# Optimization experiments

Hardware: AMD Instinct MI355X
Metric: run time of the kernel (lower is better)

## Reference

```python
import jax, jax.numpy as jnp
import numpy as np

H = W = 512
IN_DIM = 3
WIDTH = 64
N_LAYERS = 4
M1 = M2 = 20
FC_DIM = 128
OUT_DIM = 1


def setup_inputs() -> dict:
    key = jax.random.key(0)
    ks = jax.random.split(key, 12)
    s = 1.0 / (WIDTH * WIDTH)
    return {
        "x": jax.random.normal(ks[0], (H, W, IN_DIM), jnp.float32),
        "fc0_w": jax.random.normal(ks[1], (WIDTH, IN_DIM), jnp.float32) * 0.1,
        "fc0_b": jnp.zeros((WIDTH,), jnp.float32),
        "sw1_r": jax.random.normal(ks[2], (N_LAYERS, WIDTH, WIDTH, M1, M2), jnp.float32) * s,
        "sw1_i": jax.random.normal(ks[3], (N_LAYERS, WIDTH, WIDTH, M1, M2), jnp.float32) * s,
        "sw2_r": jax.random.normal(ks[4], (N_LAYERS, WIDTH, WIDTH, M1, M2), jnp.float32) * s,
        "sw2_i": jax.random.normal(ks[5], (N_LAYERS, WIDTH, WIDTH, M1, M2), jnp.float32) * s,
        "conv_w": jax.random.normal(ks[6], (N_LAYERS, WIDTH, WIDTH), jnp.float32) * 0.1,
        "conv_b": jnp.zeros((N_LAYERS, WIDTH), jnp.float32),
        "fc1_w": jax.random.normal(ks[7], (FC_DIM, WIDTH), jnp.float32) * 0.1,
        "fc1_b": jnp.zeros((FC_DIM,), jnp.float32),
        "fc2_w": jax.random.normal(ks[8], (OUT_DIM, FC_DIM), jnp.float32) * 0.1,
        "fc2_b": jnp.zeros((OUT_DIM,), jnp.float32),
    }


def _spectral_conv(v, w1, w2):
    # v: (C, H, W); w1, w2: (C_in, C_out, M1, M2) complex64
    xf = jnp.fft.rfft2(v)  # (C, H, W//2+1) complex64
    out_ft = jnp.zeros((w1.shape[1], H, W // 2 + 1), jnp.complex64)
    top = jnp.einsum("ixy,ioxy->oxy", xf[:, :M1, :M2], w1)
    bot = jnp.einsum("ixy,ioxy->oxy", xf[:, -M1:, :M2], w2)
    out_ft = out_ft.at[:, :M1, :M2].set(top).at[:, -M1:, :M2].set(bot)
    return jnp.fft.irfft2(out_ft, s=(H, W))


def reference(x, fc0_w, fc0_b, sw1_r, sw1_i, sw2_r, sw2_i, conv_w, conv_b,
              fc1_w, fc1_b, fc2_w, fc2_b):
    v = jnp.transpose(x, (2, 0, 1))  # (in_dim, H, W)
    # fc0 applied pointwise over the grid (double_vmap Linear on channel axis)
    v = jnp.einsum("chw,oc->ohw", v, fc0_w) + fc0_b[:, None, None]
    for i in range(N_LAYERS):
        w1 = (sw1_r[i] + 1j * sw1_i[i]).astype(jnp.complex64)
        w2 = (sw2_r[i] + 1j * sw2_i[i]).astype(jnp.complex64)
        x1 = _spectral_conv(v, w1, w2)
        x2 = jnp.einsum("chw,oc->ohw", v, conv_w[i]) + conv_b[i][:, None, None]
        v = jnp.tanh(x1 + x2)
    v = jnp.tanh(jnp.einsum("chw,oc->ohw", v, fc1_w) + fc1_b[:, None, None])
    v = jnp.einsum("chw,oc->ohw", v, fc2_w) + fc2_b[:, None, None]
    return jnp.transpose(v, (1, 2, 0))  # (H, W, out_dim)
```

## Files before the change

### kernel.cpp

```cpp
#include <hip/hip_runtime.h>
#include <math.h>

typedef unsigned short u16;
typedef __attribute__((ext_vector_type(8))) short short8;
typedef __attribute__((ext_vector_type(8))) short bf16x8;
typedef __attribute__((ext_vector_type(4))) unsigned short us4;
typedef __attribute__((ext_vector_type(2))) unsigned short us2;
typedef __attribute__((ext_vector_type(8))) unsigned short us8;
typedef __attribute__((ext_vector_type(4))) float f32x4;

#define NP (512*512)
#define MFMA16 __builtin_amdgcn_mfma_f32_16x16x32_bf16

#define TWH   0u
#define TWL   49152u
#define T2H   98304u
#define T2L   163840u
#define THC2H 229376u
#define THC2L 278528u
#define THS2H 327680u
#define THS2L 376832u
#define THCAH 425984u
#define THCAL 491520u
#define THSAH 557056u
#define THSAL 622592u
#define THSNH 688128u
#define THSNL 753664u
#define CFH   819200u
#define CFL   851968u
#define F1H   884736u
#define F1L   901120u
#define XWH   917504u
#define XWL   4063232u
#define XFP   7208960u
#define YPART 8028160u
#define YRH   8847360u
#define YRL   9011200u
#define YIH   9175040u
#define YIL   9338880u
#define ZH    9502720u
#define ZL    13697024u
#define VH    17891328u
#define VL    51445760u

__device__ __forceinline__ u16 brnd(float x){
    unsigned u = __float_as_uint(x);
    unsigned r = (u + 0x7FFFu + ((u>>16)&1u)) >> 16;
    return (u16)r;
}
__device__ __forceinline__ float fbf(u16 h){ return __uint_as_float(((unsigned)h)<<16); }
__device__ __forceinline__ void bsplit(float x, u16& h, u16& l){
    h = brnd(x); l = brnd(x - fbf(h));
}
__device__ __forceinline__ float tanhfast(float x){
    x = fminf(10.f, fmaxf(-10.f, x));
    float e = __expf(2.f*x);
    return (e-1.f)/(e+1.f);
}

__global__ void k_setup(char* wsb, const float* __restrict__ convw, const float* __restrict__ fc1w){
    int i = blockIdx.x*256 + threadIdx.x;
    const float c2pi = 6.283185307179586f/512.0f;
    if (i < 24576){
        int e=i&7, lane=(i>>3)&63, g=i>>9; int nt=g%3;
        int k = (g/3)*32 + ((lane>>4)<<3) + e;
        int n = nt*16 + (lane&15);
        float v=0.f;
        if(n<40){int kx=n>>1; float a=c2pi*(float)((kx*k)&511); v=(n&1)?-sinf(a):cosf(a);}
        u16 h,l; bsplit(v,h,l);
        ((u16*)(wsb+TWH))[i]=h; ((u16*)(wsb+TWL))[i]=l;
    } else if (i < 57344){
        int j2=i-24576;
        int e=j2&7, lane=(j2>>3)&63, g=j2>>9; int ks=g&1, wt=g>>1;
        int j = ks*32 + ((lane>>4)<<3) + e;
        int w = wt*16 + (lane&15);
        float v=0.f;
        if(j<40){int kx=j>>1; float a=c2pi*(float)((kx*w)&511); v=(j&1)?-sinf(a):cosf(a);}
        u16 h,l; bsplit(v,h,l);
        ((u16*)(wsb+T2H))[j2]=h; ((u16*)(wsb+T2L))[j2]=l;
    } else if (i < 81920){
        int j2 = i-57344;
        int m=j2>>9, hh=j2&511;
        float vc=0.f,vs=0.f;
        if(m<40){int ky=(m<20)?m:(472+m); float a=c2pi*(float)((ky*hh)&511); vc=cosf(a); vs=sinf(a);}
        u16 h,l;
        bsplit(vc,h,l); ((u16*)(wsb+THC2H))[j2]=h; ((u16*)(wsb+THC2L))[j2]=l;
        bsplit(vs,h,l); ((u16*)(wsb+THS2H))[j2]=h; ((u16*)(wsb+THS2L))[j2]=l;
    } else if (i < 114688){
        int j2 = i-81920;
        int hh=j2>>6, m=j2&63;
        float vc=0.f,vs=0.f;
        if(m<40){int ky=(m<20)?m:(472+m); float a=c2pi*(float)((ky*hh)&511); vc=cosf(a); vs=sinf(a);}
        u16 h,l;
        bsplit(vc,h,l);  ((u16*)(wsb+THCAH))[j2]=h; ((u16*)(wsb+THCAL))[j2]=l;
        bsplit(vs,h,l);  ((u16*)(wsb+THSAH))[j2]=h; ((u16*)(wsb+THSAL))[j2]=l;
        bsplit(-vs,h,l); ((u16*)(wsb+THSNH))[j2]=h; ((u16*)(wsb+THSNL))[j2]=l;
    } else {
        int j = i - 114688;
        if (j < 16384){
            int e=j&7, lane=(j>>3)&63, g=j>>9;
            int mt=g&3, ks=(g>>2)&1, L=g>>3;
            int o = mt*16+(lane&15), c = ks*32+((lane>>4)<<3)+e;
            float v = convw[L*4096 + o*64 + c];
            u16 h,l; bsplit(v,h,l);
            ((u16*)(wsb+CFH))[j]=h; ((u16*)(wsb+CFL))[j]=l;
        } else {
            int j2=j-16384;
            int e=j2&7, lane=(j2>>3)&63, g=j2>>9;
            int mt=g&7, ks=g>>3;
            int f = mt*16+(lane&15), c = ks*32+((lane>>4)<<3)+e;
            float v = fc1w[f*64+c];
            u16 h,l; bsplit(v,h,l);
            ((u16*)(wsb+F1H))[j2]=h; ((u16*)(wsb+F1L))[j2]=l;
        }
    }
}

__global__ __launch_bounds__(256) void k_fc0(const float* __restrict__ x,
    const float* __restrict__ w, const float* __restrict__ b,
    u16* __restrict__ vh, u16* __restrict__ vl){
    __shared__ float xs[1024*3];
    __shared__ float ws3[192], bs[64];
    int t = threadIdx.x;
    size_t pb = (size_t)blockIdx.x*1024;
    const float4* xg = (const float4*)(x + pb*3);
    float4* xs4 = (float4*)xs;
    #pragma unroll
    for (int k=0;k<3;k++) xs4[t + k*256] = xg[t + k*256];
    if (t<192) ws3[t]=w[t];
    if (t<64) bs[t]=b[t];
    __syncthreads();
    int p0 = t*4;
    float X0[4],X1[4],X2[4];
    #pragma unroll
    for(int e=0;e<4;e++){X0[e]=xs[(p0+e)*3];X1[e]=xs[(p0+e)*3+1];X2[e]=xs[(p0+e)*3+2];}
    for (int c=0;c<64;c++){
        float w0=ws3[c*3],w1=ws3[c*3+1],w2=ws3[c*3+2],bc=bs[c];
        us4 sh, sl;
        #pragma unroll
        for(int e=0;e<4;e++){
            float v = w0*X0[e]+w1*X1[e]+w2*X2[e]+bc;
            u16 hh,ll; bsplit(v,hh,ll); sh[e]=hh; sl[e]=ll;
        }
        *(us4*)(vh + (size_t)c*NP + pb + p0) = sh;
        *(us4*)(vl + (size_t)c*NP + pb + p0) = sl;
    }
}

__global__ __launch_bounds__(256) void k_f1(const u16* __restrict__ vh, const u16* __restrict__ vl,
    const u16* __restrict__ twh, const u16* __restrict__ twl,
    u16* __restrict__ xwh, u16* __restrict__ xwl){
    int lane = threadIdx.x & 63, wv = threadIdx.x >> 6;
    int rowa = blockIdx.x*64 + wv*16 + (lane&15);
    const u16* ah = vh + (size_t)rowa*512 + ((lane>>4)<<3);
    const u16* al = vl + (size_t)rowa*512 + ((lane>>4)<<3);
    f32x4 acc[3];
    #pragma unroll
    for (int nt = 0; nt < 3; ++nt) acc[nt] = (f32x4){0.f,0.f,0.f,0.f};
    #pragma unroll 2
    for (int kk = 0; kk < 16; ++kk){
        bf16x8 Ah = *reinterpret_cast<const bf16x8*>(ah + kk*32);
        bf16x8 Al = *reinterpret_cast<const bf16x8*>(al + kk*32);
        bf16x8 Bh[3], Bl[3];
        #pragma unroll
        for (int nt = 0; nt < 3; ++nt){
            size_t bo = ((size_t)(kk*3+nt)*64 + lane)*8;
            Bh[nt] = *reinterpret_cast<const bf16x8*>(twh + bo);
            Bl[nt] = *reinterpret_cast<const bf16x8*>(twl + bo);
        }
        #pragma unroll
        for (int nt = 0; nt < 3; ++nt){
            acc[nt] = MFMA16(Ah, Bh[nt], acc[nt], 0,0,0);
            acc[nt] = MFMA16(Ah, Bl[nt], acc[nt], 0,0,0);
            acc[nt] = MFMA16(Al, Bh[nt], acc[nt], 0,0,0);
        }
    }
    int r0 = blockIdx.x*64 + wv*16 + ((lane>>4)<<2);
    int c = r0>>9, h0 = r0&511;
    int colj = lane&15;
    #pragma unroll
    for (int nt = 0; nt < 3; ++nt){
        int j = nt*16 + colj;
        us4 uh, ul;
        #pragma unroll
        for (int rg = 0; rg < 4; ++rg){
            u16 hh,ll; bsplit(acc[nt][rg],hh,ll); uh[rg]=hh; ul[rg]=ll;
        }
        size_t off = ((size_t)j*64 + c)*512 + h0;
        *(us4*)(xwh + off) = uh;
        *(us4*)(xwl + off) = ul;
    }
}

__global__ __launch_bounds__(256) void k_f2(const char* __restrict__ wsb, float* __restrict__ xfP){
    int b = blockIdx.x;
    int kx = b/6, r = b%6, mt = r>>1, kh = r&1;
    int lane = threadIdx.x&63, wv = threadIdx.x>>6;
    const u16* thch=(const u16*)(wsb+THC2H); const u16* thcl=(const u16*)(wsb+THC2L);
    const u16* thsh=(const u16*)(wsb+THS2H); const u16* thsl=(const u16*)(wsb+THS2L);
    const u16* xwh=(const u16*)(wsb+XWH);   const u16* xwl=(const u16*)(wsb+XWL);
    f32x4 aA=(f32x4){0,0,0,0}, aB=aA, aC=aA, aD=aA;
    int g8 = (lane>>4)<<3;
    int mrow = lane&15;
    int cB = wv*16 + (lane&15);
    size_t bre = ((size_t)(2*kx)*64 + cB)*512;
    size_t bim = ((size_t)(2*kx+1)*64 + cB)*512;
    for (int kk = kh*8; kk < kh*8+8; ++kk){
        int hof = kk*32 + g8;
        bf16x8 XRh = *reinterpret_cast<const bf16x8*>(xwh + bre + hof);
        bf16x8 XRl = *reinterpret_cast<const bf16x8*>(xwl + bre + hof);
        bf16x8 XIh = *reinterpret_cast<const bf16x8*>(xwh + bim + hof);
        bf16x8 XIl = *reinterpret_cast<const bf16x8*>(xwl + bim + hof);
        size_t ao = (size_t)(mt*16+mrow)*512 + hof;
        bf16x8 Ch = *reinterpret_cast<const bf16x8*>(thch+ao);
        bf16x8 Cl = *reinterpret_cast<const bf16x8*>(thcl+ao);
        bf16x8 Sh = *reinterpret_cast<const bf16x8*>(thsh+ao);
        bf16x8 Sl = *reinterpret_cast<const bf16x8*>(thsl+ao);
        aA=MFMA16(Ch,XRh,aA,0,0,0); aA=MFMA16(Ch,XRl,aA,0,0,0); aA=MFMA16(Cl,XRh,aA,0,0,0);
        aB=MFMA16(Sh,XIh,aB,0,0,0); aB=MFMA16(Sh,XIl,aB,0,0,0); aB=MFMA16(Sl,XIh,aB,0,0,0);
        aC=MFMA16(Ch,XIh,aC,0,0,0); aC=MFMA16(Ch,XIl,aC,0,0,0); aC=MFMA16(Cl,XIh,aC,0,0,0);
        aD=MFMA16(Sh,XRh,aD,0,0,0); aD=MFMA16(Sh,XRl,aD,0,0,0); aD=MFMA16(Sl,XRh,aD,0,0,0);
    }
    #pragma unroll
    for (int rg=0;rg<4;rg++){
        int m = mt*16 + ((lane>>4)<<2) + rg;
        if (m < 40){
            float re = aA[rg]+aB[rg];
            float im = aC[rg]-aD[rg];
            size_t xo = ((size_t)kh*64 + cB)*1600 + (size_t)(m*20+kx)*2;
            xfP[xo] = re; xfP[xo+1] = im;
        }
    }
}

__global__ __launch_bounds__(256) void k_mix(const float* __restrict__ w1r,const float* __restrict__ w1i,
    const float* __restrict__ w2r,const float* __restrict__ w2i,
    const float* __restrict__ xfP, float* __restrict__ ypart){
    __shared__ float xs[2][800];
    int b = blockIdx.x;
    int iseg = b>>7, half = (b>>6)&1, o = b&63;
    int t = threadIdx.x;
    const float* wr = (half? w2r : w1r) + o*400;
    const float* wi = (half? w2i : w1i) + o*400;
    const float* xp0 = xfP + half*800;
    const float* xp1 = xfP + (size_t)64*1600 + half*800;
    int i0 = iseg*32;
    {
        const float* a = xp0 + (size_t)i0*1600; const float* c = xp1 + (size_t)i0*1600;
        xs[0][t]=a[t]+c[t]; xs[0][t+256]=a[t+256]+c[t+256];
        if (t<288) xs[0][t+512]=a[t+512]+c[t+512];
    }
    int p1 = t, p2 = t+256; bool has2 = (p2<400);
    float ar1=0,ai1=0,ar2=0,ai2=0;
    size_t wof = (size_t)i0*25600;
    float wAr1=wr[wof+p1], wAi1=wi[wof+p1];
    float wAr2=0,wAi2=0;
    if(has2){ wAr2=wr[wof+p2]; wAi2=wi[wof+p2]; }
    __syncthreads();
    for (int ii=0; ii<32; ++ii){
        int cur = ii&1;
        if (ii<31){
            int i = i0+ii+1;
            const float* a = xp0 + (size_t)i*1600; const float* c = xp1 + (size_t)i*1600;
            float* d = xs[cur^1];
            d[t]=a[t]+c[t]; d[t+256]=a[t+256]+c[t+256];
            if(t<288) d[t+512]=a[t+512]+c[t+512];
        }
        float wBr1=0,wBi1=0,wBr2=0,wBi2=0;
        if (ii<31){
            size_t wo2 = (size_t)(i0+ii+1)*25600;
            wBr1=wr[wo2+p1]; wBi1=wi[wo2+p1];
            if(has2){ wBr2=wr[wo2+p2]; wBi2=wi[wo2+p2]; }
        }
        float xr=xs[cur][2*p1], xi=xs[cur][2*p1+1];
        ar1 += xr*wAr1 - xi*wAi1; ai1 += xr*wAi1 + xi*wAr1;
        if (has2){
            float xr2=xs[cur][2*p2], xi2=xs[cur][2*p2+1];
            ar2 += xr2*wAr2 - xi2*wAi2; ai2 += xr2*wAi2 + xi2*wAr2;
        }
        wAr1=wBr1; wAi1=wBi1; wAr2=wBr2; wAi2=wBi2;
        __syncthreads();
    }
    int mode1 = half*400 + p1;
    size_t y1 = ((size_t)(iseg*800 + mode1)*64 + o)*2;
    ypart[y1]=ar1; ypart[y1+1]=ai1;
    if (has2){
        int mode2 = half*400 + p2;
        size_t y2 = ((size_t)(iseg*800 + mode2)*64 + o)*2;
        ypart[y2]=ar2; ypart[y2+1]=ai2;
    }
}

__global__ void k_mixred(const float* __restrict__ ypart, char* wsb){
    int g = blockIdx.x*256+threadIdx.x;
    int m = g&63, o=(g>>6)&63, kx=g>>12;
    float vr=0.f, vi=0.f;
    if (m<40){
        int mode = m*20+kx;
        size_t i0 = ((size_t)mode*64+o)*2;
        size_t i1 = ((size_t)(800+mode)*64+o)*2;
        float sc = (kx==0?1.f:2.f)*(1.f/262144.f);
        vr = (ypart[i0]+ypart[i1])*sc;
        vi = (ypart[i0+1]+ypart[i1+1])*sc;
    }
    u16 h,l; size_t yo = ((size_t)kx*64+o)*64+m;
    bsplit(vr,h,l); ((u16*)(wsb+YRH))[yo]=h; ((u16*)(wsb+YRL))[yo]=l;
    bsplit(vi,h,l); ((u16*)(wsb+YIH))[yo]=h; ((u16*)(wsb+YIL))[yo]=l;
}

__global__ __launch_bounds__(128) void k_i1(const char* __restrict__ wsb,
    u16* __restrict__ zh, u16* __restrict__ zl){
    int b = blockIdx.x; int kx = b>>4, hb = b&15;
    int lane = threadIdx.x&63, wv = threadIdx.x>>6;
    const u16* thcAh=(const u16*)(wsb+THCAH); const u16* thcAl=(const u16*)(wsb+THCAL);
    const u16* thsAh=(const u16*)(wsb+THSAH); const u16* thsAl=(const u16*)(wsb+THSAL);
    const u16* thsnh=(const u16*)(wsb+THSNH); const u16* thsnl=(const u16*)(wsb+THSNL);
    const u16* yrh=(const u16*)(wsb+YRH); const u16* yrl=(const u16*)(wsb+YRL);
    const u16* yih=(const u16*)(wsb+YIH); const u16* yil=(const u16*)(wsb+YIL);
    f32x4 aR[4], aI[4];
    #pragma unroll
    for(int nt=0;nt<4;nt++){aR[nt]=(f32x4){0,0,0,0}; aI[nt]=aR[nt];}
    int g8 = (lane>>4)<<3;
    int hrow = hb*32 + wv*16 + (lane&15);
    #pragma unroll
    for (int ks=0; ks<2; ++ks){
        size_t ao = (size_t)hrow*64 + ks*32 + g8;
        bf16x8 Ch=*reinterpret_cast<const bf16x8*>(thcAh+ao);
        bf16x8 Cl=*reinterpret_cast<const bf16x8*>(thcAl+ao);
        bf16x8 Sh=*reinterpret_cast<const bf16x8*>(thsAh+ao);
        bf16x8 Sl=*reinterpret_cast<const bf16x8*>(thsAl+ao);
        bf16x8 Nh=*reinterpret_cast<const bf16x8*>(thsnh+ao);
        bf16x8 Nl=*reinterpret_cast<const bf16x8*>(thsnl+ao);
        #pragma unroll
        for (int nt=0; nt<4; ++nt){
            int o = nt*16+(lane&15);
            size_t bo = ((size_t)kx*64+o)*64 + ks*32 + g8;
            bf16x8 Rh=*reinterpret_cast<const bf16x8*>(yrh+bo);
            bf16x8 Rl=*reinterpret_cast<const bf16x8*>(yrl+bo);
            bf16x8 Ih=*reinterpret_cast<const bf16x8*>(yih+bo);
            bf16x8 Il=*reinterpret_cast<const bf16x8*>(yil+bo);
            aR[nt]=MFMA16(Ch,Rh,aR[nt],0,0,0); aR[nt]=MFMA16(Ch,Rl,aR[nt],0,0,0); aR[nt]=MFMA16(Cl,Rh,aR[nt],0,0,0);
            aR[nt]=MFMA16(Nh,Ih,aR[nt],0,0,0); aR[nt]=MFMA16(Nh,Il,aR[nt],0,0,0); aR[nt]=MFMA16(Nl,Ih,aR[nt],0,0,0);
            aI[nt]=MFMA16(Sh,Rh,aI[nt],0,0,0); aI[nt]=MFMA16(Sh,Rl,aI[nt],0,0,0); aI[nt]=MFMA16(Sl,Rh,aI[nt],0,0,0);
            aI[nt]=MFMA16(Ch,Ih,aI[nt],0,0,0); aI[nt]=MFMA16(Ch,Il,aI[nt],0,0,0); aI[nt]=MFMA16(Cl,Ih,aI[nt],0,0,0);
        }
    }
    #pragma unroll
    for (int nt=0;nt<4;nt++)
        #pragma unroll
        for (int rg=0;rg<4;rg++){
            int h = hb*32 + wv*16 + ((lane>>4)<<2) + rg;
            int o = nt*16+(lane&15);
            size_t za = ((size_t)h*64+o)*64 + 2*kx;
            u16 h1,l1,h2,l2;
            bsplit(aR[nt][rg],h1,l1); bsplit(aI[nt][rg],h2,l2);
            us2 sh={h1,h2}, sl={l1,l2};
            *(us2*)(zh+za)=sh; *(us2*)(zl+za)=sl;
        }
}

#define SWZ(c,p) ((c) ^ (((p)&7)<<3))
__global__ __launch_bounds__(256) void k_sct(u16* __restrict__ vh, u16* __restrict__ vl,
    const char* __restrict__ wsb, int L, const float* __restrict__ cb,
    const u16* __restrict__ zh, const u16* __restrict__ zl){
    __shared__ u16 sh_[4096];
    __shared__ u16 sl_[4096];
    __shared__ unsigned so_[64*68];
    int t = threadIdx.x, lane = t&63, wv = t>>6;
    int h = blockIdx.x>>3, pb = (blockIdx.x&7)<<6;
    size_t gbase = (size_t)h*512 + pb;
    const u16* cfh=(const u16*)(wsb+CFH); const u16* cfl=(const u16*)(wsb+CFL);
    const u16* t2h=(const u16*)(wsb+T2H); const u16* t2l=(const u16*)(wsb+T2L);
    int g = lane>>4;
    int colp = wv*16 + (lane&15);
    int wt = (pb>>4) + wv;
    int cst = t>>2, p0s=(t&3)<<4;
    short8 a0 = *(const short8*)(vh + (size_t)cst*NP + gbase + p0s);
    short8 a1 = *(const short8*)(vh + (size_t)cst*NP + gbase + p0s+8);
    short8 b0 = *(const short8*)(vl + (size_t)cst*NP + gbase + p0s);
    short8 b1 = *(const short8*)(vl + (size_t)cst*NP + gbase + p0s+8);
    bf16x8 cA0[4][2], zA0[4][2], tB0[2];
    #pragma unroll
    for (int mt=0;mt<4;mt++){
        size_t fo = (size_t)(((L*2+0)*4+mt)*64 + lane)*8;
        cA0[mt][0] = *reinterpret_cast<const bf16x8*>(cfh+fo);
        cA0[mt][1] = *reinterpret_cast<const bf16x8*>(cfl+fo);
        size_t ao = (((size_t)h*64 + mt*16+(lane&15))*64) + (g<<3);
        zA0[mt][0] = *reinterpret_cast<const bf16x8*>(zh+ao);
        zA0[mt][1] = *reinterpret_cast<const bf16x8*>(zl+ao);
    }
    {
        size_t bo = ((size_t)(wt*2+0)*64 + lane)*8;
        tB0[0] = *reinterpret_cast<const bf16x8*>(t2h+bo);
        tB0[1] = *reinterpret_cast<const bf16x8*>(t2l+bo);
    }
    #pragma unroll
    for (int e=0;e<8;e++){
        sh_[(p0s+e)*64 + SWZ(cst,p0s+e)] = (u16)a0[e];
        sh_[(p0s+8+e)*64 + SWZ(cst,p0s+8+e)] = (u16)a1[e];
        sl_[(p0s+e)*64 + SWZ(cst,p0s+e)] = (u16)b0[e];
        sl_[(p0s+8+e)*64 + SWZ(cst,p0s+8+e)] = (u16)b1[e];
    }
    __syncthreads();
    f32x4 acc[4];
    #pragma unroll
    for (int mt=0;mt<4;mt++) acc[mt]=(f32x4){0,0,0,0};
    {
        int so = colp*64 + ((g ^ (colp&7))<<3);
        bf16x8 Bh = *reinterpret_cast<const bf16x8*>(sh_+so);
        bf16x8 Bl = *reinterpret_cast<const bf16x8*>(sl_+so);
        #pragma unroll
        for (int mt=0;mt<4;mt++){
            acc[mt]=MFMA16(cA0[mt][0],Bh,acc[mt],0,0,0);
            acc[mt]=MFMA16(cA0[mt][0],Bl,acc[mt],0,0,0);
            acc[mt]=MFMA16(cA0[mt][1],Bh,acc[mt],0,0,0);
        }
    }
    bf16x8 cA1[4][2], zA1[4][2], tB1[2];
    #pragma unroll
    for (int mt=0;mt<4;mt++){
        size_t fo = (size_t)(((L*2+1)*4+mt)*64 + lane)*8;
        cA1[mt][0] = *reinterpret_cast<const bf16x8*>(cfh+fo);
        cA1[mt][1] = *reinterpret_cast<const bf16x8*>(cfl+fo);
        size_t ao = (((size_t)h*64 + mt*16+(lane&15))*64) + 32 + (g<<3);
        zA1[mt][0] = *reinterpret_cast<const bf16x8*>(zh+ao);
        zA1[mt][1] = *reinterpret_cast<const bf16x8*>(zl+ao);
    }
    {
        size_t bo = ((size_t)(wt*2+1)*64 + lane)*8;
        tB1[0] = *reinterpret_cast<const bf16x8*>(t2h+bo);
        tB1[1] = *reinterpret_cast<const bf16x8*>(t2l+bo);
    }
    #pragma unroll
    for (int mt=0;mt<4;mt++){
        acc[mt]=MFMA16(zA0[mt][0],tB0[0],acc[mt],0,0,0);
        acc[mt]=MFMA16(zA0[mt][0],tB0[1],acc[mt],0,0,0);
        acc[mt]=MFMA16(zA0[mt][1],tB0[0],acc[mt],0,0,0);
    }
    {
        int so = colp*64 + (((4+g) ^ (colp&7))<<3);
        bf16x8 Bh = *reinterpret_cast<const bf16x8*>(sh_+so);
        bf16x8 Bl = *reinterpret_cast<const bf16x8*>(sl_+so);
        #pragma unroll
        for (int mt=0;mt<4;mt++){
            acc[mt]=MFMA16(cA1[mt][0],Bh,acc[mt],0,0,0);
            acc[mt]=MFMA16(cA1[mt][0],Bl,acc[mt],0,0,0);
            acc[mt]=MFMA16(cA1[mt][1],Bh,acc[mt],0,0,0);
        }
    }
    #pragma unroll
    for (int mt=0;mt<4;mt++){
        acc[mt]=MFMA16(zA1[mt][0],tB1[0],acc[mt],0,0,0);
        acc[mt]=MFMA16(zA1[mt][0],tB1[1],acc[mt],0,0,0);
        acc[mt]=MFMA16(zA1[mt][1],tB1[0],acc[mt],0,0,0);
    }
    #pragma unroll
    for (int mt=0;mt<4;mt++){
        float4 cbv = *reinterpret_cast<const float4*>(cb + mt*16 + (g<<2));
        float cba[4] = {cbv.x, cbv.y, cbv.z, cbv.w};
        #pragma unroll
        for (int rg=0;rg<4;rg++){
            int o = mt*16 + (g<<2) + rg;
            float val = tanhfast(acc[mt][rg] + cba[rg]);
            u16 hh,ll; bsplit(val,hh,ll);
            so_[o*68 + colp] = (unsigned)hh | ((unsigned)ll<<16);
        }
    }
    __syncthreads();
    {
        int o = t>>2, p0 = (t&3)<<4;
        const uint4* sp = reinterpret_cast<const uint4*>(so_ + o*68 + p0);
        uint4 u0 = sp[0], u1 = sp[1], u2 = sp[2], u3 = sp[3];
        us8 h0, h1, l0, l1;
        h0[0]=(u16)u0.x; l0[0]=(u16)(u0.x>>16);
        h0[1]=(u16)u0.y; l0[1]=(u16)(u0.y>>16);
        h0[2]=(u16)u0.z; l0[2]=(u16)(u0.z>>16);
        h0[3]=(u16)u0.w; l0[3]=(u16)(u0.w>>16);
        h0[4]=(u16)u1.x; l0[4]=(u16)(u1.x>>16);
        h0[5]=(u16)u1.y; l0[5]=(u16)(u1.y>>16);
        h0[6]=(u16)u1.z; l0[6]=(u16)(u1.z>>16);
        h0[7]=(u16)u1.w; l0[7]=(u16)(u1.w>>16);
        h1[0]=(u16)u2.x; l1[0]=(u16)(u2.x>>16);
        h1[1]=(u16)u2.y; l1[1]=(u16)(u2.y>>16);
        h1[2]=(u16)u2.z; l1[2]=(u16)(u2.z>>16);
        h1[3]=(u16)u2.w; l1[3]=(u16)(u2.w>>16);
        h1[4]=(u16)u3.x; l1[4]=(u16)(u3.x>>16);
        h1[5]=(u16)u3.y; l1[5]=(u16)(u3.y>>16);
        h1[6]=(u16)u3.z; l1[6]=(u16)(u3.z>>16);
        h1[7]=(u16)u3.w; l1[7]=(u16)(u3.w>>16);
        size_t go = (size_t)o*NP + gbase + p0;
        *(us8*)(vh+go)   = h0;
        *(us8*)(vh+go+8) = h1;
        *(us8*)(vl+go)   = l0;
        *(us8*)(vl+go+8) = l1;
    }
}

__global__ __launch_bounds__(256) void k_fc12(const u16* __restrict__ vh, const u16* __restrict__ vl,
    const char* __restrict__ wsb, const float* __restrict__ b1,
    const float* __restrict__ w2, const float* __restrict__ b2, float* __restrict__ out){
    __shared__ u16 sh_[4096];
    __shared__ u16 sl_[4096];
    int t = threadIdx.x, lane = t&63, wv = t>>6;
    size_t pb = (size_t)blockIdx.x*64;
    {
        int c = t>>2, p0=(t&3)<<4;
        short8 a0 = *(const short8*)(vh + (size_t)c*NP + pb + p0);
        short8 a1 = *(const short8*)(vh + (size_t)c*NP + pb + p0+8);
        short8 b0 = *(const short8*)(vl + (size_t)c*NP + pb + p0);
        short8 b1 = *(const short8*)(vl + (size_t)c*NP + pb + p0+8);
        #pragma unroll
        for (int e=0;e<8;e++){
            sh_[(p0+e)*64 + SWZ(c,p0+e)] = (u16)a0[e];
            sh_[(p0+8+e)*64 + SWZ(c,p0+8+e)] = (u16)a1[e];
            sl_[(p0+e)*64 + SWZ(c,p0+e)] = (u16)b0[e];
            sl_[(p0+8+e)*64 + SWZ(c,p0+8+e)] = (u16)b1[e];
        }
    }
    __syncthreads();
    f32x4 acc[8];
    #pragma unroll
    for (int mt=0;mt<8;mt++) acc[mt]=(f32x4){0,0,0,0};
    int colp = wv*16 + (lane&15);
    int g = lane>>4;
    const u16* f1h=(const u16*)(wsb+F1H); const u16* f1l=(const u16*)(wsb+F1L);
    #pragma unroll
    for (int ks=0;ks<2;ks++){
        bf16x8 A[8][2];
        #pragma unroll
        for (int mt=0;mt<8;mt++){
            size_t fo = (size_t)((ks*8+mt)*64 + lane)*8;
            A[mt][0] = *reinterpret_cast<const bf16x8*>(f1h+fo);
            A[mt][1] = *reinterpret_cast<const bf16x8*>(f1l+fo);
        }
        int o8 = ks*4+g;
        int so = colp*64 + ((o8 ^ (colp&7))<<3);
        bf16x8 Bh = *reinterpret_cast<const bf16x8*>(sh_+so);
        bf16x8 Bl = *reinterpret_cast<const bf16x8*>(sl_+so);
        #pragma unroll
        for (int mt=0;mt<8;mt++){
            acc[mt]=MFMA16(A[mt][0],Bh,acc[mt],0,0,0);
            acc[mt]=MFMA16(A[mt][0],Bl,acc[mt],0,0,0);
            acc[mt]=MFMA16(A[mt][1],Bh,acc[mt],0,0,0);
        }
    }
    float s = 0.f;
    #pragma unroll
    for (int mt=0;mt<8;mt++)
        #pragma unroll
        for (int rg=0;rg<4;rg++){
            int f = mt*16 + (g<<2) + rg;
            s += w2[f] * tanhfast(acc[mt][rg] + b1[f]);
        }
    s += __shfl_xor(s, 16);
    s += __shfl_xor(s, 32);
    if (lane < 16) out[pb + wv*16 + lane] = s + b2[0];
}

extern "C" void kernel_launch(void* const* d_in, const int* in_sizes, int n_in,
                              void* d_out, int out_size, void* d_ws, size_t ws_size,
                              hipStream_t stream) {
    const float* x     = (const float*)d_in[0];
    const float* fc0w  = (const float*)d_in[1];
    const float* fc0b  = (const float*)d_in[2];
    const float* sw1r  = (const float*)d_in[3];
    const float* sw1i  = (const float*)d_in[4];
    const float* sw2r  = (const float*)d_in[5];
    const float* sw2i  = (const float*)d_in[6];
    const float* convw = (const float*)d_in[7];
    const float* convb = (const float*)d_in[8];
    const float* fc1w  = (const float*)d_in[9];
    const float* fc1b  = (const float*)d_in[10];
    const float* fc2w  = (const float*)d_in[11];
    const float* fc2b  = (const float*)d_in[12];
    char* wsb = (char*)d_ws;
    float* out = (float*)d_out;

    u16* twh = (u16*)(wsb+TWH); u16* twl = (u16*)(wsb+TWL);
    u16* xwh = (u16*)(wsb+XWH); u16* xwl = (u16*)(wsb+XWL);
    float* xfP = (float*)(wsb+XFP);
    float* ypart = (float*)(wsb+YPART);
    u16* zh = (u16*)(wsb+ZH); u16* zl = (u16*)(wsb+ZL);
    u16* vh = (u16*)(wsb+VH); u16* vl = (u16*)(wsb+VL);

    k_setup<<<544, 256, 0, stream>>>(wsb, convw, fc1w);
    k_fc0<<<256, 256, 0, stream>>>(x, fc0w, fc0b, vh, vl);
    for (int L = 0; L < 4; ++L){
        size_t so = (size_t)L * 64 * 64 * 400;
        k_f1<<<512, 256, 0, stream>>>(vh, vl, twh, twl, xwh, xwl);
        k_f2<<<120, 256, 0, stream>>>(wsb, xfP);
        k_mix<<<256, 256, 0, stream>>>(sw1r+so, sw1i+so, sw2r+so, sw2i+so, xfP, ypart);
        k_mixred<<<320, 256, 0, stream>>>(ypart, wsb);
        k_i1<<<320, 128, 0, stream>>>(wsb, zh, zl);
        k_sct<<<4096, 256, 0, stream>>>(vh, vl, wsb, L, convb + (size_t)L*64, zh, zl);
    }
    k_fc12<<<4096, 256, 0, stream>>>(vh, vl, wsb, fc1b, fc2w, fc2b, out);
}
```

Baseline: 729.4 us.

## Double rows per wave in k_f1 and alias shared buffers in k_sct

k_f1 now has each wave compute two 16-row tiles that share the same twiddle B fragments. This halves the B loads per output and halves the grid to 256 blocks. Separately, k_sct places the output staging buffer on top of the input shared buffers, with an added barrier, so shared memory drops from about 33KB to 17KB and occupancy can rise. The risks are fewer blocks in k_f1, which may underfill the CUs, and an extra __syncthreads in k_sct.

```diff
diff --git a/kernel.cpp b/kernel.cpp
--- a/kernel.cpp
+++ b/kernel.cpp
@@ -151,16 +151,20 @@
     const u16* __restrict__ twh, const u16* __restrict__ twl,
     u16* __restrict__ xwh, u16* __restrict__ xwl){
     int lane = threadIdx.x & 63, wv = threadIdx.x >> 6;
-    int rowa = blockIdx.x*64 + wv*16 + (lane&15);
-    const u16* ah = vh + (size_t)rowa*512 + ((lane>>4)<<3);
-    const u16* al = vl + (size_t)rowa*512 + ((lane>>4)<<3);
-    f32x4 acc[3];
-    #pragma unroll
-    for (int nt = 0; nt < 3; ++nt) acc[nt] = (f32x4){0.f,0.f,0.f,0.f};
+    int r0a = blockIdx.x*128 + wv*16;
+    int r1a = r0a + 64;
+    int rl = lane&15;
+    const u16* ah0 = vh + (size_t)(r0a+rl)*512 + ((lane>>4)<<3);
+    const u16* al0 = vl + (size_t)(r0a+rl)*512 + ((lane>>4)<<3);
+    const u16* ah1 = vh + (size_t)(r1a+rl)*512 + ((lane>>4)<<3);
+    const u16* al1 = vl + (size_t)(r1a+rl)*512 + ((lane>>4)<<3);
+    f32x4 acc[2][3];
+    #pragma unroll
+    for (int tt = 0; tt < 2; ++tt)
+        #pragma unroll
+        for (int nt = 0; nt < 3; ++nt) acc[tt][nt] = (f32x4){0.f,0.f,0.f,0.f};
     #pragma unroll 2
     for (int kk = 0; kk < 16; ++kk){
-        bf16x8 Ah = *reinterpret_cast<const bf16x8*>(ah + kk*32);
-        bf16x8 Al = *reinterpret_cast<const bf16x8*>(al + kk*32);
         bf16x8 Bh[3], Bl[3];
         #pragma unroll
         for (int nt = 0; nt < 3; ++nt){
@@ -168,27 +172,37 @@
             Bh[nt] = *reinterpret_cast<const bf16x8*>(twh + bo);
             Bl[nt] = *reinterpret_cast<const bf16x8*>(twl + bo);
         }
+        bf16x8 Ah0 = *reinterpret_cast<const bf16x8*>(ah0 + kk*32);
+        bf16x8 Al0 = *reinterpret_cast<const bf16x8*>(al0 + kk*32);
+        bf16x8 Ah1 = *reinterpret_cast<const bf16x8*>(ah1 + kk*32);
+        bf16x8 Al1 = *reinterpret_cast<const bf16x8*>(al1 + kk*32);
         #pragma unroll
         for (int nt = 0; nt < 3; ++nt){
-            acc[nt] = MFMA16(Ah, Bh[nt], acc[nt], 0,0,0);
-            acc[nt] = MFMA16(Ah, Bl[nt], acc[nt], 0,0,0);
-            acc[nt] = MFMA16(Al, Bh[nt], acc[nt], 0,0,0);
-        }
-    }
-    int r0 = blockIdx.x*64 + wv*16 + ((lane>>4)<<2);
-    int c = r0>>9, h0 = r0&511;
+            acc[0][nt] = MFMA16(Ah0, Bh[nt], acc[0][nt], 0,0,0);
+            acc[0][nt] = MFMA16(Ah0, Bl[nt], acc[0][nt], 0,0,0);
+            acc[0][nt] = MFMA16(Al0, Bh[nt], acc[0][nt], 0,0,0);
+            acc[1][nt] = MFMA16(Ah1, Bh[nt], acc[1][nt], 0,0,0);
+            acc[1][nt] = MFMA16(Ah1, Bl[nt], acc[1][nt], 0,0,0);
+            acc[1][nt] = MFMA16(Al1, Bh[nt], acc[1][nt], 0,0,0);
+        }
+    }
     int colj = lane&15;
     #pragma unroll
-    for (int nt = 0; nt < 3; ++nt){
-        int j = nt*16 + colj;
-        us4 uh, ul;
-        #pragma unroll
-        for (int rg = 0; rg < 4; ++rg){
-            u16 hh,ll; bsplit(acc[nt][rg],hh,ll); uh[rg]=hh; ul[rg]=ll;
-        }
-        size_t off = ((size_t)j*64 + c)*512 + h0;
-        *(us4*)(xwh + off) = uh;
-        *(us4*)(xwl + off) = ul;
+    for (int tt = 0; tt < 2; ++tt){
+        int r0 = (tt ? r1a : r0a) + ((lane>>4)<<2);
+        int c = r0>>9, h0 = r0&511;
+        #pragma unroll
+        for (int nt = 0; nt < 3; ++nt){
+            int j = nt*16 + colj;
+            us4 uh, ul;
+            #pragma unroll
+            for (int rg = 0; rg < 4; ++rg){
+                u16 hh,ll; bsplit(acc[tt][nt][rg],hh,ll); uh[rg]=hh; ul[rg]=ll;
+            }
+            size_t off = ((size_t)j*64 + c)*512 + h0;
+            *(us4*)(xwh + off) = uh;
+            *(us4*)(xwl + off) = ul;
+        }
     }
 }
 
@@ -363,9 +377,10 @@
 __global__ __launch_bounds__(256) void k_sct(u16* __restrict__ vh, u16* __restrict__ vl,
     const char* __restrict__ wsb, int L, const float* __restrict__ cb,
     const u16* __restrict__ zh, const u16* __restrict__ zl){
-    __shared__ u16 sh_[4096];
-    __shared__ u16 sl_[4096];
-    __shared__ unsigned so_[64*68];
+    __shared__ __align__(16) char smem[17408];
+    u16* sh_ = (u16*)smem;
+    u16* sl_ = (u16*)(smem + 8192);
+    unsigned* so_ = (unsigned*)smem;
     int t = threadIdx.x, lane = t&63, wv = t>>6;
     int h = blockIdx.x>>3, pb = (blockIdx.x&7)<<6;
     size_t gbase = (size_t)h*512 + pb;
@@ -454,6 +469,7 @@
         acc[mt]=MFMA16(zA1[mt][0],tB1[1],acc[mt],0,0,0);
         acc[mt]=MFMA16(zA1[mt][1],tB1[0],acc[mt],0,0,0);
     }
+    __syncthreads();
     #pragma unroll
     for (int mt=0;mt<4;mt++){
         float4 cbv = *reinterpret_cast<const float4*>(cb + mt*16 + (g<<2));
@@ -587,7 +603,7 @@
     k_fc0<<<256, 256, 0, stream>>>(x, fc0w, fc0b, vh, vl);
     for (int L = 0; L < 4; ++L){
         size_t so = (size_t)L * 64 * 64 * 400;
-        k_f1<<<512, 256, 0, stream>>>(vh, vl, twh, twl, xwh, xwl);
+        k_f1<<<256, 256, 0, stream>>>(vh, vl, twh, twl, xwh, xwl);
         k_f2<<<120, 256, 0, stream>>>(wsb, xfP);
         k_mix<<<256, 256, 0, stream>>>(sw1r+so, sw1i+so, sw2r+so, sw2i+so, xfP, ypart);
         k_mixred<<<320, 256, 0, stream>>>(ypart, wsb);
```

New measurement: 727.6 us. Within noise of the previous version (-0.2%).
